# Performance work log

Hardware: AMD Instinct MI355X
Metric: run time of the kernel (lower is better)

The kernel has to match this reference:

```python
import jax, jax.numpy as jnp
import numpy as np

D_K = 128
SCALE = float(np.sqrt(D_K))

def setup_inputs() -> dict:
    key = jax.random.key(0)
    k1, k2, k3, k4 = jax.random.split(key, 4)
    B, S, D = 16, 2048, 128
    Q = jax.random.normal(k1, (B, S, D), dtype=jnp.float32)
    K = jax.random.normal(k2, (B, S, D), dtype=jnp.float32)
    V = jax.random.normal(k3, (B, S, D), dtype=jnp.float32)
    mask = jax.random.randint(k4, (B, 1, S), 0, 2).astype(jnp.bool_)
    return {"Q": Q, "K": K, "V": V, "mask": mask}

def reference(Q, K, V, mask):
    # scores: (B, Sq, Sk)
    scores = jnp.einsum("bqd,bkd->bqk", Q, K) / SCALE
    allow = jnp.broadcast_to(mask, scores.shape)
    neg = jnp.finfo(scores.dtype).min
    scores = jnp.where(allow, scores, neg)
    query_has_keys = jnp.any(allow, axis=-1, keepdims=True)  # (B, Sq, 1)
    scores = jnp.where(query_has_keys, scores, 0.0)
    attn_weights = jax.nn.softmax(scores, axis=-1)
    attn_weights = jnp.where(allow, attn_weights, 0.0)
    # dropout p=0.0 -> identity
    output = jnp.einsum("bqk,bkd->bqd", attn_weights, V)
    output = jnp.where(query_has_keys, output, 0.0)
    return output, attn_weights
```

## Files before the change

kernel.cpp:

```cpp
#include <hip/hip_runtime.h>

#define BB 16
#define SS 2048
#define DD 128
#define CE (0.08838834764831845f * 1.4426950408889634f)

typedef __attribute__((ext_vector_type(4))) float f32x4;
typedef __attribute__((ext_vector_type(8))) short short8;
typedef __attribute__((ext_vector_type(4))) unsigned short us4;
typedef __attribute__((ext_vector_type(8))) unsigned short us8;

__device__ inline unsigned short f2bf(float f) {
    unsigned u = __float_as_uint(f);
    u += 0x7fffu + ((u >> 16) & 1u);
    return (unsigned short)(u >> 16);
}

__device__ inline int swzA(int row, int col) {
    int byteoff = (row << 8) + ((col >> 3) << 4);
    byteoff ^= (row & 7) << 4;
    return (byteoff >> 1) + (col & 7);
}
__device__ inline int swzB(int row, int col) {
    int byteoff = (row << 7) + ((col >> 3) << 4);
    byteoff ^= (row & 7) << 4;
    return (byteoff >> 1) + (col & 7);
}

__global__ __launch_bounds__(256) void prep_kernel(
    const float* __restrict__ Q, const float* __restrict__ K,
    const float* __restrict__ V, const int* __restrict__ mask,
    unsigned short* __restrict__ Qb, unsigned short* __restrict__ Kb,
    unsigned short* __restrict__ VT, float* __restrict__ maskAdd)
{
    __shared__ unsigned short tile[64 * 136];
    int b = blockIdx.y, k0 = blockIdx.x << 6;
    int t = threadIdx.x;
    const size_t base = ((size_t)b * SS + k0) * DD;

    for (int i = 0; i < 8; ++i) {
        int f4 = (i << 8) + t;
        f32x4 q = reinterpret_cast<const f32x4*>(Q + base)[f4];
        f32x4 k = reinterpret_cast<const f32x4*>(K + base)[f4];
        us4 qh, kh;
        for (int j = 0; j < 4; ++j) { qh[j] = f2bf(q[j]); kh[j] = f2bf(k[j]); }
        reinterpret_cast<us4*>(Qb + base)[f4] = qh;
        reinterpret_cast<us4*>(Kb + base)[f4] = kh;
    }
    if (t < 64)
        maskAdd[(size_t)b * SS + k0 + t] =
            mask[(size_t)b * SS + k0 + t] ? 0.0f : __int_as_float(0xff800000);

    for (int i = 0; i < 8; ++i) {
        int f4 = (i << 8) + t;
        int k  = f4 >> 5;
        int n  = (f4 & 31) << 2;
        f32x4 v = reinterpret_cast<const f32x4*>(V + base)[f4];
        us4 h;
        for (int j = 0; j < 4; ++j) h[j] = f2bf(v[j]);
        *reinterpret_cast<us4*>(&tile[k * 136 + n]) = h;
    }
    __syncthreads();
    unsigned short* outp = VT + (size_t)b * DD * SS;
    for (int i = 0; i < 4; ++i) {
        int id = (i << 8) + t;
        int n  = id >> 3;
        int c8 = id & 7;
        us8 o;
        for (int j = 0; j < 8; ++j) o[j] = tile[((c8 << 3) + j) * 136 + n];
        *reinterpret_cast<us8*>(&outp[(size_t)n * SS + k0 + (c8 << 3)]) = o;
    }
}

__global__ __launch_bounds__(256, 2) void flashA_kernel(
    const unsigned short* __restrict__ Qb, const unsigned short* __restrict__ Kb,
    const unsigned short* __restrict__ VT, const float* __restrict__ maskAdd,
    float* __restrict__ Op0, float* __restrict__ Op1, float* __restrict__ Lp)
{
    __shared__ unsigned short Ks[2][64 * 128];
    __shared__ unsigned short VTs[2][128 * 64];
    __shared__ unsigned short Ps[4 * 1024];

    const int id = blockIdx.x;
    const int xcd = id & 7, j = id >> 3;
    const int b   = (xcd << 1) | (j >> 5);
    const int rem = j & 31;
    const int half = rem >> 4, qb = rem & 15;
    const int q0 = qb << 7;
    const int kvbase = half << 10;

    const int t = threadIdx.x, lane = t & 63, w = t >> 6;
    const int lr = lane & 15, lg = lane >> 4;

    const unsigned short* Kbb = Kb + (size_t)b * SS * DD;
    const unsigned short* Vbb = VT + (size_t)b * DD * SS;
    const float* Mb = maskAdd + (size_t)b * SS;

    const unsigned short* Qp = Qb + ((size_t)b * SS + q0 + w * 32) * DD;
    short8 qf[2][4];
    for (int m = 0; m < 2; ++m)
        for (int kb = 0; kb < 4; ++kb)
            qf[m][kb] = *reinterpret_cast<const short8*>(
                Qp + (size_t)(m * 16 + lr) * DD + kb * 32 + lg * 8);

    f32x4 oacc[2][8] = {};
    float rsum[2] = {0.f, 0.f};
    unsigned short* Pw = &Ps[w * 1024];

    us8 kstg[4], vstg[4];
#define LOADTILE(kv)                                                             \
    for (int i = 0; i < 4; ++i) {                                                \
        int f = i * 256 + t;                                                     \
        kstg[i] = *reinterpret_cast<const us8*>(                                 \
            Kbb + (size_t)((kv) + (f >> 4)) * DD + ((f & 15) << 3));             \
        vstg[i] = *reinterpret_cast<const us8*>(                                 \
            Vbb + (size_t)(f >> 3) * SS + (kv) + ((f & 7) << 3));                \
    }
#define WRITETILE(bf)                                                            \
    for (int i = 0; i < 4; ++i) {                                                \
        int f = i * 256 + t;                                                     \
        *reinterpret_cast<us8*>(&Ks[bf][swzA(f >> 4, (f & 15) << 3)]) = kstg[i]; \
        *reinterpret_cast<us8*>(&VTs[bf][swzB(f >> 3, (f & 7) << 3)]) = vstg[i]; \
    }

    LOADTILE(kvbase);
    WRITETILE(0);

    for (int kt = 0; kt < 16; ++kt) {
        const int cur = kt & 1;
        const int kv0 = kvbase + (kt << 6);
        if (kt + 1 < 16) { LOADTILE(kv0 + 64); }
        __syncthreads();

        f32x4 sacc[2][4] = {};
        __builtin_amdgcn_s_setprio(1);
        for (int kb = 0; kb < 4; ++kb) {
            short8 kf[4];
            for (int n = 0; n < 4; ++n)
                kf[n] = *reinterpret_cast<const short8*>(
                    &Ks[cur][swzA(n * 16 + lr, kb * 32 + lg * 8)]);
            for (int n = 0; n < 4; ++n)
                for (int m = 0; m < 2; ++m)
                    sacc[m][n] = __builtin_amdgcn_mfma_f32_16x16x32_bf16(
                        kf[n], qf[m][kb], sacc[m][n], 0, 0, 0);
        }
        __builtin_amdgcn_s_setprio(0);

        for (int h = 0; h < 2; ++h) {
            for (int nl = 0; nl < 2; ++nl) {
                int n = h * 2 + nl;
                f32x4 ma = *reinterpret_cast<const f32x4*>(Mb + kv0 + n * 16 + lg * 4);
                for (int m = 0; m < 2; ++m) {
                    us4 hh;
                    for (int r = 0; r < 4; ++r) {
                        float p = __builtin_amdgcn_exp2f(fmaf(sacc[m][n][r], CE, ma[r]));
                        rsum[m] += p;
                        hh[r] = f2bf(p);
                    }
                    *reinterpret_cast<us4*>(&Pw[swzB(lr, m * 32 + nl * 16 + lg * 4)]) = hh;
                }
            }
            asm volatile("s_waitcnt lgkmcnt(0)" ::: "memory");
            __builtin_amdgcn_sched_barrier(0);

            short8 pf[2];
            for (int m = 0; m < 2; ++m)
                pf[m] = *reinterpret_cast<const short8*>(&Pw[swzB(lr, m * 32 + lg * 8)]);
            __builtin_amdgcn_s_setprio(1);
            for (int nd = 0; nd < 8; ++nd) {
                short8 vf = *reinterpret_cast<const short8*>(
                    &VTs[cur][swzB(nd * 16 + lr, h * 32 + lg * 8)]);
                for (int m = 0; m < 2; ++m)
                    oacc[m][nd] = __builtin_amdgcn_mfma_f32_16x16x32_bf16(
                        pf[m], vf, oacc[m][nd], 0, 0, 0);
            }
            __builtin_amdgcn_s_setprio(0);
        }

        if (kt + 1 < 16) { WRITETILE(cur ^ 1); }
    }
#undef LOADTILE
#undef WRITETILE

    for (int m = 0; m < 2; ++m) {
        rsum[m] += __shfl_xor(rsum[m], 16, 64);
        rsum[m] += __shfl_xor(rsum[m], 32, 64);
    }
    if (lane < 16)
        for (int m = 0; m < 2; ++m)
            Lp[(size_t)half * BB * SS + (size_t)b * SS + q0 + w * 32 + m * 16 + lane] = rsum[m];

    float* Op = half ? Op1 : Op0;
    float* Og = Op + ((size_t)b * SS + q0 + w * 32) * DD;
    for (int m = 0; m < 2; ++m)
        for (int nd = 0; nd < 8; ++nd)
            for (int r = 0; r < 4; ++r)
                Og[(size_t)(m * 16 + lg * 4 + r) * DD + nd * 16 + lr] = oacc[m][nd][r];
}

__global__ __launch_bounds__(256) void combine_kernel(
    const float* __restrict__ Op0, const float* __restrict__ Op1,
    const float* __restrict__ Lp, float* __restrict__ O, float* __restrict__ l2il)
{
    int i = blockIdx.x * 256 + threadIdx.x;
    int row = i >> 5;
    float L = Lp[row] + Lp[BB * SS + row];
    float il = L > 0.f ? 1.f / L : 0.f;
    f32x4 a = reinterpret_cast<const f32x4*>(Op0)[i];
    f32x4 c = reinterpret_cast<const f32x4*>(Op1)[i];
    f32x4 o;
    for (int r = 0; r < 4; ++r) o[r] = (a[r] + c[r]) * il;
    reinterpret_cast<f32x4*>(O)[i] = o;
    if ((i & 31) == 0)
        l2il[row] = L > 0.f ? -__builtin_amdgcn_logf(L) : __int_as_float(0xff800000);
}

__global__ __launch_bounds__(256, 4) void pstore_kernel(
    const unsigned short* __restrict__ Qb, const unsigned short* __restrict__ Kb,
    const float* __restrict__ maskAdd, const float* __restrict__ l2il,
    float* __restrict__ P)
{
    __shared__ unsigned short Ks[2][64 * 128];

    const int id = blockIdx.x;
    const int xcd = id & 7, j = id >> 3;
    const int b   = (xcd << 1) | (j >> 6);
    const int rem = j & 63;
    const int kvq = rem >> 4, qb = rem & 15;
    const int q0 = qb << 7, kvbase = kvq << 9;

    const int t = threadIdx.x, lane = t & 63, w = t >> 6;
    const int lr = lane & 15, lg = lane >> 4;

    const unsigned short* Kbb = Kb + (size_t)b * SS * DD;
    const float* Mb = maskAdd + (size_t)b * SS;

    const unsigned short* Qp = Qb + ((size_t)b * SS + q0 + w * 32) * DD;
    short8 qf[2][4];
    for (int m = 0; m < 2; ++m)
        for (int kb = 0; kb < 4; ++kb)
            qf[m][kb] = *reinterpret_cast<const short8*>(
                Qp + (size_t)(m * 16 + lr) * DD + kb * 32 + lg * 8);

    float lil[2];
    for (int m = 0; m < 2; ++m)
        lil[m] = l2il[(size_t)b * SS + q0 + w * 32 + m * 16 + lr];

    us8 kstg[4];
#define LOADK(kv)                                                                \
    for (int i = 0; i < 4; ++i) {                                                \
        int f = i * 256 + t;                                                     \
        kstg[i] = *reinterpret_cast<const us8*>(                                 \
            Kbb + (size_t)((kv) + (f >> 4)) * DD + ((f & 15) << 3));             \
    }
#define WRITEK(bf)                                                               \
    for (int i = 0; i < 4; ++i) {                                                \
        int f = i * 256 + t;                                                     \
        *reinterpret_cast<us8*>(&Ks[bf][swzA(f >> 4, (f & 15) << 3)]) = kstg[i]; \
    }

    LOADK(kvbase);
    WRITEK(0);

    for (int kt = 0; kt < 8; ++kt) {
        const int cur = kt & 1;
        const int kv0 = kvbase + (kt << 6);
        if (kt + 1 < 8) { LOADK(kv0 + 64); }
        __syncthreads();

        f32x4 sacc[2][4] = {};
        for (int kb = 0; kb < 4; ++kb) {
            short8 kf[4];
            for (int n = 0; n < 4; ++n)
                kf[n] = *reinterpret_cast<const short8*>(
                    &Ks[cur][swzA(n * 16 + lr, kb * 32 + lg * 8)]);
            for (int n = 0; n < 4; ++n)
                for (int m = 0; m < 2; ++m)
                    sacc[m][n] = __builtin_amdgcn_mfma_f32_16x16x32_bf16(
                        kf[n], qf[m][kb], sacc[m][n], 0, 0, 0);
        }

        for (int m = 0; m < 2; ++m) {
            float* Pp = P + ((size_t)b * SS + q0 + w * 32 + m * 16 + lr) * SS + kv0;
            for (int n = 0; n < 4; ++n) {
                f32x4 ma = *reinterpret_cast<const f32x4*>(Mb + kv0 + n * 16 + lg * 4);
                f32x4 out;
                for (int r = 0; r < 4; ++r)
                    out[r] = __builtin_amdgcn_exp2f(
                        fmaf(sacc[m][n][r], CE, ma[r]) + lil[m]);
                *reinterpret_cast<f32x4*>(Pp + n * 16 + lg * 4) = out;
            }
        }

        if (kt + 1 < 8) { WRITEK(cur ^ 1); }
    }
#undef LOADK
#undef WRITEK
}

__global__ __launch_bounds__(256) void qk_exp_kernel(
    const float* __restrict__ Q, const float* __restrict__ Kin,
    const int* __restrict__ mask, float* __restrict__ P)
{
    __shared__ unsigned short Qs[128 * 128];
    __shared__ unsigned short Ks[128 * 128];
    const int b  = blockIdx.z;
    const int m0 = blockIdx.y << 7;
    const int n0 = blockIdx.x << 7;
    const int t  = threadIdx.x;
    const float* Qp = Q   + ((size_t)b * SS + m0) * DD;
    const float* Kp = Kin + ((size_t)b * SS + n0) * DD;
    for (int i = 0; i < 16; ++i) {
        int f4  = (i << 8) + t;
        int row = f4 >> 5;
        int col = (f4 & 31) << 2;
        f32x4 q = reinterpret_cast<const f32x4*>(Qp)[f4];
        f32x4 k = reinterpret_cast<const f32x4*>(Kp)[f4];
        us4 qh, kh;
        for (int jj = 0; jj < 4; ++jj) { qh[jj] = f2bf(q[jj]); kh[jj] = f2bf(k[jj]); }
        *reinterpret_cast<us4*>(&Qs[swzA(row, col)]) = qh;
        *reinterpret_cast<us4*>(&Ks[swzA(row, col)]) = kh;
    }
    __syncthreads();
    const int lane = t & 63, wid = t >> 6;
    const int wr = wid >> 1, wc = wid & 1;
    const int lr = lane & 15, lg = lane >> 4;
    f32x4 acc[4][4] = {};
    for (int kb = 0; kb < 4; ++kb) {
        short8 a[4], bq[4];
        int kcol = (kb << 5) + (lg << 3);
        for (int m = 0; m < 4; ++m)
            a[m] = *reinterpret_cast<const short8*>(&Qs[swzA((wr << 6) + (m << 4) + lr, kcol)]);
        for (int n = 0; n < 4; ++n)
            bq[n] = *reinterpret_cast<const short8*>(&Ks[swzA((wc << 6) + (n << 4) + lr, kcol)]);
        for (int m = 0; m < 4; ++m)
            for (int n = 0; n < 4; ++n)
                acc[m][n] = __builtin_amdgcn_mfma_f32_16x16x32_bf16(a[m], bq[n], acc[m][n], 0, 0, 0);
    }
    const int* am = mask + (size_t)b * SS;
    for (int n = 0; n < 4; ++n) {
        int col = n0 + (wc << 6) + (n << 4) + lr;
        bool allow = am[col] != 0;
        for (int m = 0; m < 4; ++m) {
            int rowb = m0 + (wr << 6) + (m << 4) + (lg << 2);
            float* Pp = P + ((size_t)b * SS + rowb) * SS + col;
            for (int r = 0; r < 4; ++r) {
                float p = allow ? __expf(acc[m][n][r] * 0.08838834764831845f) : 0.0f;
                Pp[(size_t)r * SS] = p;
            }
        }
    }
}

__global__ __launch_bounds__(256) void norm_kernel(float* __restrict__ P)
{
    int row  = (blockIdx.x << 2) + (threadIdx.x >> 6);
    int lane = threadIdx.x & 63;
    float* Pr = P + (size_t)row * SS;
    f32x4 v[8];
    float sum = 0.f;
    for (int i = 0; i < 8; ++i) {
        v[i] = reinterpret_cast<f32x4*>(Pr)[(i << 6) + lane];
        sum += v[i][0] + v[i][1] + v[i][2] + v[i][3];
    }
    for (int off = 1; off < 64; off <<= 1) sum += __shfl_xor(sum, off, 64);
    float inv = sum > 0.f ? 1.f / sum : 0.f;
    for (int i = 0; i < 8; ++i) {
        f32x4 wv = v[i];
        for (int jj = 0; jj < 4; ++jj) wv[jj] *= inv;
        reinterpret_cast<f32x4*>(Pr)[(i << 6) + lane] = wv;
    }
}

__global__ __launch_bounds__(256) void pv_fallback_kernel(
    const float* __restrict__ P, const float* __restrict__ V, float* __restrict__ O)
{
    __shared__ unsigned short Ws[64 * 64];
    const int b  = blockIdx.y;
    const int m0 = blockIdx.x << 6;
    const int t  = threadIdx.x, lane = t & 63, wid = t >> 6;
    const int wr = wid >> 1, wc = wid & 1;
    const int lr = lane & 15, lg = lane >> 4;
    const float* Pg = P + ((size_t)b * SS + m0) * SS;
    f32x4 acc[2][4] = {};
    for (int k0 = 0; k0 < SS; k0 += 64) {
        __syncthreads();
        for (int i = 0; i < 4; ++i) {
            int f4  = (i << 8) + t;
            int row = f4 >> 4;
            int col = (f4 & 15) << 2;
            f32x4 wv = *reinterpret_cast<const f32x4*>(Pg + (size_t)row * SS + k0 + col);
            us4 h;
            for (int jj = 0; jj < 4; ++jj) h[jj] = f2bf(wv[jj]);
            *reinterpret_cast<us4*>(&Ws[swzB(row, col)]) = h;
        }
        __syncthreads();
        for (int kk = 0; kk < 64; kk += 32) {
            short8 a[2], bv[4];
            int kcol = kk + (lg << 3);
            for (int m = 0; m < 2; ++m)
                a[m] = *reinterpret_cast<const short8*>(&Ws[swzB((wr << 5) + (m << 4) + lr, kcol)]);
            for (int n = 0; n < 4; ++n) {
                int col = (wc << 6) + (n << 4) + lr;
                const float* vp = V + ((size_t)b * SS + k0 + kcol) * DD + col;
                short8 x;
                for (int jj = 0; jj < 8; ++jj) x[jj] = (short)f2bf(vp[(size_t)jj * DD]);
                bv[n] = x;
            }
            for (int m = 0; m < 2; ++m)
                for (int n = 0; n < 4; ++n)
                    acc[m][n] = __builtin_amdgcn_mfma_f32_16x16x32_bf16(a[m], bv[n], acc[m][n], 0, 0, 0);
        }
    }
    float* Og = O + ((size_t)b * SS + m0) * DD;
    for (int m = 0; m < 2; ++m)
        for (int n = 0; n < 4; ++n)
            for (int r = 0; r < 4; ++r)
                Og[(size_t)((wr << 5) + (m << 4) + (lg << 2) + r) * DD
                   + (wc << 6) + (n << 4) + lr] = acc[m][n][r];
}

extern "C" void kernel_launch(void* const* d_in, const int* in_sizes, int n_in,
                              void* d_out, int out_size, void* d_ws, size_t ws_size,
                              hipStream_t stream)
{
    const float* Q  = (const float*)d_in[0];
    const float* K  = (const float*)d_in[1];
    const float* V  = (const float*)d_in[2];
    const int* mask = (const int*)d_in[3];
    float* O = (float*)d_out;
    float* P = O + (size_t)BB * SS * DD;

    const size_t nE = (size_t)BB * SS * DD;
    const size_t need = 3 * nE * sizeof(unsigned short)
                      + 4 * (size_t)BB * SS * sizeof(float) + 256;

    if (ws_size >= need) {
        unsigned short* Qb = (unsigned short*)d_ws;
        unsigned short* Kb = Qb + nE;
        unsigned short* VT = Kb + nE;
        float* maskAdd = (float*)(VT + nE);
        float* Lp      = maskAdd + (size_t)BB * SS;
        float* l2il    = Lp + 2 * (size_t)BB * SS;
        float* Op0 = P;
        float* Op1 = P + nE;

        prep_kernel<<<dim3(SS / 64, BB), 256, 0, stream>>>(Q, K, V, mask, Qb, Kb, VT, maskAdd);
        flashA_kernel<<<512, 256, 0, stream>>>(Qb, Kb, VT, maskAdd, Op0, Op1, Lp);
        combine_kernel<<<4096, 256, 0, stream>>>(Op0, Op1, Lp, O, l2il);
        pstore_kernel<<<1024, 256, 0, stream>>>(Qb, Kb, maskAdd, l2il, P);
    } else {
        qk_exp_kernel<<<dim3(SS / 128, SS / 128, BB), 256, 0, stream>>>(Q, K, mask, P);
        norm_kernel<<<(BB * SS) / 4, 256, 0, stream>>>(P);
        pv_fallback_kernel<<<dim3(SS / 64, BB), 256, 0, stream>>>(P, V, O);
    }
}
```

Measured before the change: 138.8 us.

## Fuse split-KV combine into flash kernel via atomic last-block-finishes pattern

Measured after the change: 231.3 us. +66.7%, slower.

```diff
diff --git a/kernel.cpp b/kernel.cpp
--- a/kernel.cpp
+++ b/kernel.cpp
@@ -75,11 +75,13 @@
 __global__ __launch_bounds__(256, 2) void flashA_kernel(
     const unsigned short* __restrict__ Qb, const unsigned short* __restrict__ Kb,
     const unsigned short* __restrict__ VT, const float* __restrict__ maskAdd,
-    float* __restrict__ Op0, float* __restrict__ Op1, float* __restrict__ Lp)
+    float* __restrict__ Op0, float* __restrict__ Op1, float* __restrict__ Lp,
+    float* __restrict__ O, int* __restrict__ flags)
 {
     __shared__ unsigned short Ks[2][64 * 128];
     __shared__ unsigned short VTs[2][128 * 64];
     __shared__ unsigned short Ps[4 * 1024];
+    __shared__ int sOld;
 
     const int id = blockIdx.x;
     const int xcd = id & 7, j = id >> 3;
@@ -196,28 +198,34 @@
         for (int nd = 0; nd < 8; ++nd)
             for (int r = 0; r < 4; ++r)
                 Og[(size_t)(m * 16 + lg * 4 + r) * DD + nd * 16 + lr] = oacc[m][nd][r];
-}
-
-__global__ __launch_bounds__(256) void combine_kernel(
-    const float* __restrict__ Op0, const float* __restrict__ Op1,
-    const float* __restrict__ Lp, float* __restrict__ O, float* __restrict__ l2il)
-{
-    int i = blockIdx.x * 256 + threadIdx.x;
-    int row = i >> 5;
-    float L = Lp[row] + Lp[BB * SS + row];
-    float il = L > 0.f ? 1.f / L : 0.f;
-    f32x4 a = reinterpret_cast<const f32x4*>(Op0)[i];
-    f32x4 c = reinterpret_cast<const f32x4*>(Op1)[i];
-    f32x4 o;
-    for (int r = 0; r < 4; ++r) o[r] = (a[r] + c[r]) * il;
-    reinterpret_cast<f32x4*>(O)[i] = o;
-    if ((i & 31) == 0)
-        l2il[row] = L > 0.f ? -__builtin_amdgcn_logf(L) : __int_as_float(0xff800000);
+
+    __threadfence();
+    __syncthreads();
+    if (t == 0) sOld = atomicAdd(&flags[b * 16 + qb], 1);
+    __syncthreads();
+    if (sOld == 1) {
+        __threadfence();
+        const f32x4* PA = reinterpret_cast<const f32x4*>(Op0 + ((size_t)b * SS + q0) * DD);
+        const f32x4* PB = reinterpret_cast<const f32x4*>(Op1 + ((size_t)b * SS + q0) * DD);
+        f32x4* Of = reinterpret_cast<f32x4*>(O + ((size_t)b * SS + q0) * DD);
+        const float* L0 = Lp + (size_t)b * SS + q0;
+        const float* L1 = Lp + (size_t)BB * SS + (size_t)b * SS + q0;
+        for (int i = 0; i < 16; ++i) {
+            int idx = i * 256 + t;
+            int row = idx >> 5;
+            float L = L0[row] + L1[row];
+            float il = L > 0.f ? 1.f / L : 0.f;
+            f32x4 a = PA[idx], c = PB[idx];
+            f32x4 o;
+            for (int r = 0; r < 4; ++r) o[r] = (a[r] + c[r]) * il;
+            Of[idx] = o;
+        }
+    }
 }
 
 __global__ __launch_bounds__(256, 4) void pstore_kernel(
     const unsigned short* __restrict__ Qb, const unsigned short* __restrict__ Kb,
-    const float* __restrict__ maskAdd, const float* __restrict__ l2il,
+    const float* __restrict__ maskAdd, const float* __restrict__ Lp,
     float* __restrict__ P)
 {
     __shared__ unsigned short Ks[2][64 * 128];
@@ -243,8 +251,11 @@
                 Qp + (size_t)(m * 16 + lr) * DD + kb * 32 + lg * 8);
 
     float lil[2];
-    for (int m = 0; m < 2; ++m)
-        lil[m] = l2il[(size_t)b * SS + q0 + w * 32 + m * 16 + lr];
+    for (int m = 0; m < 2; ++m) {
+        size_t rowi = (size_t)b * SS + q0 + w * 32 + m * 16 + lr;
+        float L = Lp[rowi] + Lp[(size_t)BB * SS + rowi];
+        lil[m] = L > 0.f ? -__builtin_amdgcn_logf(L) : __int_as_float(0xff800000);
+    }
 
     us8 kstg[4];
 #define LOADK(kv)                                                                \
@@ -433,7 +444,8 @@
 
     const size_t nE = (size_t)BB * SS * DD;
     const size_t need = 3 * nE * sizeof(unsigned short)
-                      + 4 * (size_t)BB * SS * sizeof(float) + 256;
+                      + 3 * (size_t)BB * SS * sizeof(float)
+                      + 256 * sizeof(int) + 256;
 
     if (ws_size >= need) {
         unsigned short* Qb = (unsigned short*)d_ws;
@@ -441,14 +453,14 @@
         unsigned short* VT = Kb + nE;
         float* maskAdd = (float*)(VT + nE);
         float* Lp      = maskAdd + (size_t)BB * SS;
-        float* l2il    = Lp + 2 * (size_t)BB * SS;
+        int*   flags   = (int*)(Lp + 2 * (size_t)BB * SS);
         float* Op0 = P;
         float* Op1 = P + nE;
 
+        hipMemsetAsync(flags, 0, 256 * sizeof(int), stream);
         prep_kernel<<<dim3(SS / 64, BB), 256, 0, stream>>>(Q, K, V, mask, Qb, Kb, VT, maskAdd);
-        flashA_kernel<<<512, 256, 0, stream>>>(Qb, Kb, VT, maskAdd, Op0, Op1, Lp);
-        combine_kernel<<<4096, 256, 0, stream>>>(Op0, Op1, Lp, O, l2il);
-        pstore_kernel<<<1024, 256, 0, stream>>>(Qb, Kb, maskAdd, l2il, P);
+        flashA_kernel<<<512, 256, 0, stream>>>(Qb, Kb, VT, maskAdd, Op0, Op1, Lp, O, flags);
+        pstore_kernel<<<1024, 256, 0, stream>>>(Qb, Kb, maskAdd, Lp, P);
     } else {
         qk_exp_kernel<<<dim3(SS / 128, SS / 128, BB), 256, 0, stream>>>(Q, K, mask, P);
         norm_kernel<<<(BB * SS) / 4, 256, 0, stream>>>(P);
```

## Fuse flash attention, combine and probability store into one kernel per query block

Applied to the files above, without the earlier changes.

New measurement: 137.2 us. Within noise of the previous version (-1.1%).

```diff
diff --git a/kernel.cpp b/kernel.cpp
--- a/kernel.cpp
+++ b/kernel.cpp
@@ -72,10 +72,10 @@
     }
 }
 
-__global__ __launch_bounds__(256, 2) void flashA_kernel(
+__global__ __launch_bounds__(256, 2) void fused_kernel(
     const unsigned short* __restrict__ Qb, const unsigned short* __restrict__ Kb,
     const unsigned short* __restrict__ VT, const float* __restrict__ maskAdd,
-    float* __restrict__ Op0, float* __restrict__ Op1, float* __restrict__ Lp)
+    float* __restrict__ O, float* __restrict__ P)
 {
     __shared__ unsigned short Ks[2][64 * 128];
     __shared__ unsigned short VTs[2][128 * 64];
@@ -84,10 +84,7 @@
     const int id = blockIdx.x;
     const int xcd = id & 7, j = id >> 3;
     const int b   = (xcd << 1) | (j >> 5);
-    const int rem = j & 31;
-    const int half = rem >> 4, qb = rem & 15;
-    const int q0 = qb << 7;
-    const int kvbase = half << 10;
+    const int q0  = (j & 31) << 6;
 
     const int t = threadIdx.x, lane = t & 63, w = t >> 6;
     const int lr = lane & 15, lg = lane >> 4;
@@ -96,15 +93,13 @@
     const unsigned short* Vbb = VT + (size_t)b * DD * SS;
     const float* Mb = maskAdd + (size_t)b * SS;
 
-    const unsigned short* Qp = Qb + ((size_t)b * SS + q0 + w * 32) * DD;
-    short8 qf[2][4];
-    for (int m = 0; m < 2; ++m)
-        for (int kb = 0; kb < 4; ++kb)
-            qf[m][kb] = *reinterpret_cast<const short8*>(
-                Qp + (size_t)(m * 16 + lr) * DD + kb * 32 + lg * 8);
-
-    f32x4 oacc[2][8] = {};
-    float rsum[2] = {0.f, 0.f};
+    const unsigned short* Qp = Qb + ((size_t)b * SS + q0 + w * 16 + lr) * DD;
+    short8 qf[4];
+    for (int kb = 0; kb < 4; ++kb)
+        qf[kb] = *reinterpret_cast<const short8*>(Qp + kb * 32 + lg * 8);
+
+    f32x4 oacc[8] = {};
+    float rsum = 0.f;
     unsigned short* Pw = &Ps[w * 1024];
 
     us8 kstg[4], vstg[4];
@@ -122,131 +117,6 @@
         *reinterpret_cast<us8*>(&Ks[bf][swzA(f >> 4, (f & 15) << 3)]) = kstg[i]; \
         *reinterpret_cast<us8*>(&VTs[bf][swzB(f >> 3, (f & 7) << 3)]) = vstg[i]; \
     }
-
-    LOADTILE(kvbase);
-    WRITETILE(0);
-
-    for (int kt = 0; kt < 16; ++kt) {
-        const int cur = kt & 1;
-        const int kv0 = kvbase + (kt << 6);
-        if (kt + 1 < 16) { LOADTILE(kv0 + 64); }
-        __syncthreads();
-
-        f32x4 sacc[2][4] = {};
-        __builtin_amdgcn_s_setprio(1);
-        for (int kb = 0; kb < 4; ++kb) {
-            short8 kf[4];
-            for (int n = 0; n < 4; ++n)
-                kf[n] = *reinterpret_cast<const short8*>(
-                    &Ks[cur][swzA(n * 16 + lr, kb * 32 + lg * 8)]);
-            for (int n = 0; n < 4; ++n)
-                for (int m = 0; m < 2; ++m)
-                    sacc[m][n] = __builtin_amdgcn_mfma_f32_16x16x32_bf16(
-                        kf[n], qf[m][kb], sacc[m][n], 0, 0, 0);
-        }
-        __builtin_amdgcn_s_setprio(0);
-
-        for (int h = 0; h < 2; ++h) {
-            for (int nl = 0; nl < 2; ++nl) {
-                int n = h * 2 + nl;
-                f32x4 ma = *reinterpret_cast<const f32x4*>(Mb + kv0 + n * 16 + lg * 4);
-                for (int m = 0; m < 2; ++m) {
-                    us4 hh;
-                    for (int r = 0; r < 4; ++r) {
-                        float p = __builtin_amdgcn_exp2f(fmaf(sacc[m][n][r], CE, ma[r]));
-                        rsum[m] += p;
-                        hh[r] = f2bf(p);
-                    }
-                    *reinterpret_cast<us4*>(&Pw[swzB(lr, m * 32 + nl * 16 + lg * 4)]) = hh;
-                }
-            }
-            asm volatile("s_waitcnt lgkmcnt(0)" ::: "memory");
-            __builtin_amdgcn_sched_barrier(0);
-
-            short8 pf[2];
-            for (int m = 0; m < 2; ++m)
-                pf[m] = *reinterpret_cast<const short8*>(&Pw[swzB(lr, m * 32 + lg * 8)]);
-            __builtin_amdgcn_s_setprio(1);
-            for (int nd = 0; nd < 8; ++nd) {
-                short8 vf = *reinterpret_cast<const short8*>(
-                    &VTs[cur][swzB(nd * 16 + lr, h * 32 + lg * 8)]);
-                for (int m = 0; m < 2; ++m)
-                    oacc[m][nd] = __builtin_amdgcn_mfma_f32_16x16x32_bf16(
-                        pf[m], vf, oacc[m][nd], 0, 0, 0);
-            }
-            __builtin_amdgcn_s_setprio(0);
-        }
-
-        if (kt + 1 < 16) { WRITETILE(cur ^ 1); }
-    }
-#undef LOADTILE
-#undef WRITETILE
-
-    for (int m = 0; m < 2; ++m) {
-        rsum[m] += __shfl_xor(rsum[m], 16, 64);
-        rsum[m] += __shfl_xor(rsum[m], 32, 64);
-    }
-    if (lane < 16)
-        for (int m = 0; m < 2; ++m)
-            Lp[(size_t)half * BB * SS + (size_t)b * SS + q0 + w * 32 + m * 16 + lane] = rsum[m];
-
-    float* Op = half ? Op1 : Op0;
-    float* Og = Op + ((size_t)b * SS + q0 + w * 32) * DD;
-    for (int m = 0; m < 2; ++m)
-        for (int nd = 0; nd < 8; ++nd)
-            for (int r = 0; r < 4; ++r)
-                Og[(size_t)(m * 16 + lg * 4 + r) * DD + nd * 16 + lr] = oacc[m][nd][r];
-}
-
-__global__ __launch_bounds__(256) void combine_kernel(
-    const float* __restrict__ Op0, const float* __restrict__ Op1,
-    const float* __restrict__ Lp, float* __restrict__ O, float* __restrict__ l2il)
-{
-    int i = blockIdx.x * 256 + threadIdx.x;
-    int row = i >> 5;
-    float L = Lp[row] + Lp[BB * SS + row];
-    float il = L > 0.f ? 1.f / L : 0.f;
-    f32x4 a = reinterpret_cast<const f32x4*>(Op0)[i];
-    f32x4 c = reinterpret_cast<const f32x4*>(Op1)[i];
-    f32x4 o;
-    for (int r = 0; r < 4; ++r) o[r] = (a[r] + c[r]) * il;
-    reinterpret_cast<f32x4*>(O)[i] = o;
-    if ((i & 31) == 0)
-        l2il[row] = L > 0.f ? -__builtin_amdgcn_logf(L) : __int_as_float(0xff800000);
-}
-
-__global__ __launch_bounds__(256, 4) void pstore_kernel(
-    const unsigned short* __restrict__ Qb, const unsigned short* __restrict__ Kb,
-    const float* __restrict__ maskAdd, const float* __restrict__ l2il,
-    float* __restrict__ P)
-{
-    __shared__ unsigned short Ks[2][64 * 128];
-
-    const int id = blockIdx.x;
-    const int xcd = id & 7, j = id >> 3;
-    const int b   = (xcd << 1) | (j >> 6);
-    const int rem = j & 63;
-    const int kvq = rem >> 4, qb = rem & 15;
-    const int q0 = qb << 7, kvbase = kvq << 9;
-
-    const int t = threadIdx.x, lane = t & 63, w = t >> 6;
-    const int lr = lane & 15, lg = lane >> 4;
-
-    const unsigned short* Kbb = Kb + (size_t)b * SS * DD;
-    const float* Mb = maskAdd + (size_t)b * SS;
-
-    const unsigned short* Qp = Qb + ((size_t)b * SS + q0 + w * 32) * DD;
-    short8 qf[2][4];
-    for (int m = 0; m < 2; ++m)
-        for (int kb = 0; kb < 4; ++kb)
-            qf[m][kb] = *reinterpret_cast<const short8*>(
-                Qp + (size_t)(m * 16 + lr) * DD + kb * 32 + lg * 8);
-
-    float lil[2];
-    for (int m = 0; m < 2; ++m)
-        lil[m] = l2il[(size_t)b * SS + q0 + w * 32 + m * 16 + lr];
-
-    us8 kstg[4];
 #define LOADK(kv)                                                                \
     for (int i = 0; i < 4; ++i) {                                                \
         int f = i * 256 + t;                                                     \
@@ -259,41 +129,105 @@
         *reinterpret_cast<us8*>(&Ks[bf][swzA(f >> 4, (f & 15) << 3)]) = kstg[i]; \
     }
 
-    LOADK(kvbase);
-    WRITEK(0);
-
-    for (int kt = 0; kt < 8; ++kt) {
+    LOADTILE(0);
+    WRITETILE(0);
+
+    for (int kt = 0; kt < 32; ++kt) {
         const int cur = kt & 1;
-        const int kv0 = kvbase + (kt << 6);
-        if (kt + 1 < 8) { LOADK(kv0 + 64); }
+        const int kv0 = kt << 6;
+        if (kt + 1 < 32) { LOADTILE(kv0 + 64); }
         __syncthreads();
 
-        f32x4 sacc[2][4] = {};
+        f32x4 sacc[4] = {};
+        __builtin_amdgcn_s_setprio(1);
         for (int kb = 0; kb < 4; ++kb) {
             short8 kf[4];
             for (int n = 0; n < 4; ++n)
                 kf[n] = *reinterpret_cast<const short8*>(
                     &Ks[cur][swzA(n * 16 + lr, kb * 32 + lg * 8)]);
             for (int n = 0; n < 4; ++n)
-                for (int m = 0; m < 2; ++m)
-                    sacc[m][n] = __builtin_amdgcn_mfma_f32_16x16x32_bf16(
-                        kf[n], qf[m][kb], sacc[m][n], 0, 0, 0);
-        }
-
-        for (int m = 0; m < 2; ++m) {
-            float* Pp = P + ((size_t)b * SS + q0 + w * 32 + m * 16 + lr) * SS + kv0;
-            for (int n = 0; n < 4; ++n) {
-                f32x4 ma = *reinterpret_cast<const f32x4*>(Mb + kv0 + n * 16 + lg * 4);
-                f32x4 out;
-                for (int r = 0; r < 4; ++r)
-                    out[r] = __builtin_amdgcn_exp2f(
-                        fmaf(sacc[m][n][r], CE, ma[r]) + lil[m]);
-                *reinterpret_cast<f32x4*>(Pp + n * 16 + lg * 4) = out;
+                sacc[n] = __builtin_amdgcn_mfma_f32_16x16x32_bf16(
+                    kf[n], qf[kb], sacc[n], 0, 0, 0);
+        }
+        __builtin_amdgcn_s_setprio(0);
+
+        for (int n = 0; n < 4; ++n) {
+            f32x4 ma = *reinterpret_cast<const f32x4*>(Mb + kv0 + n * 16 + lg * 4);
+            us4 hh;
+            for (int r = 0; r < 4; ++r) {
+                float p = __builtin_amdgcn_exp2f(fmaf(sacc[n][r], CE, ma[r]));
+                rsum += p;
+                hh[r] = f2bf(p);
             }
-        }
-
-        if (kt + 1 < 8) { WRITEK(cur ^ 1); }
-    }
+            *reinterpret_cast<us4*>(&Pw[swzB(lr, n * 16 + lg * 4)]) = hh;
+        }
+        asm volatile("s_waitcnt lgkmcnt(0)" ::: "memory");
+        __builtin_amdgcn_sched_barrier(0);
+
+        __builtin_amdgcn_s_setprio(1);
+        for (int kb2 = 0; kb2 < 2; ++kb2) {
+            short8 pf = *reinterpret_cast<const short8*>(&Pw[swzB(lr, kb2 * 32 + lg * 8)]);
+            for (int nd = 0; nd < 8; ++nd) {
+                short8 vf = *reinterpret_cast<const short8*>(
+                    &VTs[cur][swzB(nd * 16 + lr, kb2 * 32 + lg * 8)]);
+                oacc[nd] = __builtin_amdgcn_mfma_f32_16x16x32_bf16(pf, vf, oacc[nd], 0, 0, 0);
+            }
+        }
+        __builtin_amdgcn_s_setprio(0);
+
+        if (kt + 1 < 32) { WRITETILE(cur ^ 1); }
+    }
+
+    rsum += __shfl_xor(rsum, 16, 64);
+    rsum += __shfl_xor(rsum, 32, 64);
+
+    {
+        f32x4 invq;
+        for (int r = 0; r < 4; ++r) {
+            float Lq = __shfl(rsum, 4 * lg + r, 64);
+            invq[r] = Lq > 0.f ? 1.f / Lq : 0.f;
+        }
+        float* Og = O + ((size_t)b * SS + q0 + w * 16) * DD;
+        for (int nd = 0; nd < 8; ++nd)
+            for (int r = 0; r < 4; ++r)
+                Og[(size_t)(lg * 4 + r) * DD + nd * 16 + lr] = oacc[nd][r] * invq[r];
+    }
+    const float lil = rsum > 0.f ? -__builtin_amdgcn_logf(rsum)
+                                 : __int_as_float(0xff800000);
+
+    LOADK(0);
+    WRITEK(0);
+
+    for (int kt = 0; kt < 32; ++kt) {
+        const int cur = kt & 1;
+        const int kv0 = kt << 6;
+        if (kt + 1 < 32) { LOADK(kv0 + 64); }
+        __syncthreads();
+
+        f32x4 sacc[4] = {};
+        for (int kb = 0; kb < 4; ++kb) {
+            short8 kf[4];
+            for (int n = 0; n < 4; ++n)
+                kf[n] = *reinterpret_cast<const short8*>(
+                    &Ks[cur][swzA(n * 16 + lr, kb * 32 + lg * 8)]);
+            for (int n = 0; n < 4; ++n)
+                sacc[n] = __builtin_amdgcn_mfma_f32_16x16x32_bf16(
+                    kf[n], qf[kb], sacc[n], 0, 0, 0);
+        }
+
+        float* Pp = P + ((size_t)b * SS + q0 + w * 16 + lr) * SS + kv0;
+        for (int n = 0; n < 4; ++n) {
+            f32x4 ma = *reinterpret_cast<const f32x4*>(Mb + kv0 + n * 16 + lg * 4);
+            f32x4 out;
+            for (int r = 0; r < 4; ++r)
+                out[r] = __builtin_amdgcn_exp2f(fmaf(sacc[n][r], CE, ma[r]) + lil);
+            *reinterpret_cast<f32x4*>(Pp + n * 16 + lg * 4) = out;
+        }
+
+        if (kt + 1 < 32) { WRITEK(cur ^ 1); }
+    }
+#undef LOADTILE
+#undef WRITETILE
 #undef LOADK
 #undef WRITEK
 }
@@ -433,22 +367,16 @@
 
     const size_t nE = (size_t)BB * SS * DD;
     const size_t need = 3 * nE * sizeof(unsigned short)
-                      + 4 * (size_t)BB * SS * sizeof(float) + 256;
+                      + (size_t)BB * SS * sizeof(float) + 256;
 
     if (ws_size >= need) {
         unsigned short* Qb = (unsigned short*)d_ws;
         unsigned short* Kb = Qb + nE;
         unsigned short* VT = Kb + nE;
         float* maskAdd = (float*)(VT + nE);
-        float* Lp      = maskAdd + (size_t)BB * SS;
-        float* l2il    = Lp + 2 * (size_t)BB * SS;
-        float* Op0 = P;
-        float* Op1 = P + nE;
 
         prep_kernel<<<dim3(SS / 64, BB), 256, 0, stream>>>(Q, K, V, mask, Qb, Kb, VT, maskAdd);
-        flashA_kernel<<<512, 256, 0, stream>>>(Qb, Kb, VT, maskAdd, Op0, Op1, Lp);
-        combine_kernel<<<4096, 256, 0, stream>>>(Op0, Op1, Lp, O, l2il);
-        pstore_kernel<<<1024, 256, 0, stream>>>(Qb, Kb, maskAdd, l2il, P);
+        fused_kernel<<<512, 256, 0, stream>>>(Qb, Kb, VT, maskAdd, O, P);
     } else {
         qk_exp_kernel<<<dim3(SS / 128, SS / 128, BB), 256, 0, stream>>>(Q, K, mask, P);
         norm_kernel<<<(BB * SS) / 4, 256, 0, stream>>>(P);
```
